# Kernel tuning notes

Hardware: AMD Instinct MI355X
Metric: run time of the kernel (lower is better)

The kernel has to match this reference:

```python
import jax, jax.numpy as jnp
import numpy as np

N_NODES = 50000
N_EDGES = 800000
F_IN = 128
HID = 128
HID4 = HID // 4  # 32
N_SEL = 8192


def gcn_conv(x, src, dst, norm, W, b, n_nodes):
    h = x @ W                              # [N, out]
    msg = h[src] * norm[:, None]           # gather + scale, [E+N, out]
    out = jax.ops.segment_sum(msg, dst, num_segments=n_nodes)  # scatter-add
    return out + b


def setup_inputs() -> dict:
    key = jax.random.key(0)
    ks = jax.random.split(key, 12)
    def glorot(k, shape):
        lim = np.sqrt(6.0 / (shape[0] + shape[1])).astype(np.float32)
        return jax.random.uniform(k, shape, jnp.float32, -lim, lim)
    return {
        "x": jax.random.normal(ks[0], (N_NODES, F_IN), jnp.float32),
        "edge_index": jax.random.randint(ks[1], (2, N_EDGES), 0, N_NODES, jnp.int64 if jax.config.jax_enable_x64 else jnp.int32),
        "relevant_batch_indices": jax.random.randint(ks[2], (N_SEL,), 0, N_NODES),
        "labels": jax.random.randint(ks[3], (N_SEL,), 0, 2),
        "W1": glorot(ks[4], (F_IN, HID)),   "b1": jnp.zeros((HID,), jnp.float32),
        "W2": glorot(ks[5], (HID, HID4)),   "b2": jnp.zeros((HID4,), jnp.float32),
        "W3": glorot(ks[6], (HID4, HID4)),  "b3": jnp.zeros((HID4,), jnp.float32),
        "Wl": glorot(ks[7], (HID4, 2)),     "bl": jnp.zeros((2,), jnp.float32),
    }


def reference(x, edge_index, relevant_batch_indices, labels, W1, b1, W2, b2, W3, b3, Wl, bl):
    n = x.shape[0]
    loops = jnp.arange(n, dtype=edge_index.dtype)
    src = jnp.concatenate([edge_index[0], loops])  # add self-loops
    dst = jnp.concatenate([edge_index[1], loops])
    deg = jax.ops.segment_sum(jnp.ones_like(dst, dtype=x.dtype), dst, num_segments=n)
    dis = jnp.where(deg > 0, jax.lax.rsqrt(jnp.maximum(deg, 1e-12)), 0.0)
    norm = dis[src] * dis[dst]             # [E+N]

    h = jax.nn.relu(gcn_conv(x, src, dst, norm, W1, b1, n))
    h = jax.nn.relu(gcn_conv(h, src, dst, norm, W2, b2, n))
    h = gcn_conv(h, src, dst, norm, W3, b3, n)

    logits = h[relevant_batch_indices] @ Wl + bl   # [N_SEL, 2]
    softmax_vals = jax.nn.softmax(logits, axis=1)
    lsm = jax.nn.log_softmax(logits, axis=1)
    # original slices lsm to labels length if longer; here shapes match
    lsm = lsm[: labels.shape[0]]
    return (lsm, softmax_vals)
```

## Files before the change

### kernel.cpp

```cpp
#include <hip/hip_runtime.h>
#include <hip/hip_fp16.h>

#define F_IN 128
#define HID 128
#define HID4 32
#define NPB 256
#define SRC_BITS 17
#define NBK 256
#define MAXBUCKET 256

static inline size_t alignup(size_t x) { return (x + 255) & ~(size_t)255; }

typedef _Float16 half8 __attribute__((ext_vector_type(8)));
typedef float f32x4 __attribute__((ext_vector_type(4)));

union F4H8 { float4 f; __half2 h[4]; };
union U2H4 { uint2 u; _Float16 h[4]; };


__global__ __launch_bounds__(1024) void hist_k(const int* __restrict__ dst,
                                               int* __restrict__ ghist, int ne, int n_buckets) {
    __shared__ int h[MAXBUCKET];
    const int t = threadIdx.x;
    for (int b = t; b < n_buckets; b += 1024) h[b] = 0;
    __syncthreads();
    const int chunk = (ne + NBK - 1) / NBK;
    const int beg = blockIdx.x * chunk;
    const int end = min(ne, beg + chunk);
    for (int e = beg + t; e < end; e += 1024)
        atomicAdd(&h[dst[e] / NPB], 1);
    __syncthreads();
    for (int b = t; b < n_buckets; b += 1024)
        ghist[(size_t)b * NBK + blockIdx.x] = h[b];
}


__global__ void scan_block_k(const int* __restrict__ in, int* __restrict__ out,
                             int* __restrict__ partials, int n) {
    __shared__ int tmp[256];
    int i = blockIdx.x * 256 + threadIdx.x;
    int v = (i < n) ? in[i] : 0;
    tmp[threadIdx.x] = v;
    __syncthreads();
    for (int off = 1; off < 256; off <<= 1) {
        int t = (threadIdx.x >= off) ? tmp[threadIdx.x - off] : 0;
        __syncthreads();
        tmp[threadIdx.x] += t;
        __syncthreads();
    }
    if (i < n) out[i] = tmp[threadIdx.x] - v;
    if (threadIdx.x == 255) partials[blockIdx.x] = tmp[255];
}

__global__ void scan_partials_k(int* __restrict__ partials, int nb) {
    __shared__ int tmp[256];
    int v = (threadIdx.x < nb) ? partials[threadIdx.x] : 0;
    tmp[threadIdx.x] = v;
    __syncthreads();
    for (int off = 1; off < 256; off <<= 1) {
        int t = (threadIdx.x >= off) ? tmp[threadIdx.x - off] : 0;
        __syncthreads();
        tmp[threadIdx.x] += t;
        __syncthreads();
    }
    if (threadIdx.x < nb) partials[threadIdx.x] = tmp[threadIdx.x] - v;
}

__global__ void add2_k(int* __restrict__ goff, const int* __restrict__ partials, int n) {
    int i = blockIdx.x * 256 + threadIdx.x;
    if (i < n) goff[i] += partials[i >> 8];
}


__global__ __launch_bounds__(1024) void scatter2_k(const int* __restrict__ src, const int* __restrict__ dst,
                                                   const int* __restrict__ goff,
                                                   unsigned* __restrict__ tmp, int ne, int n_buckets) {
    __shared__ int cur[MAXBUCKET];
    const int t = threadIdx.x;
    for (int b = t; b < n_buckets; b += 1024)
        cur[b] = goff[(size_t)b * NBK + blockIdx.x];
    __syncthreads();
    const int chunk = (ne + NBK - 1) / NBK;
    const int beg = blockIdx.x * chunk;
    const int end = min(ne, beg + chunk);
    for (int e = beg + t; e < end; e += 1024) {
        int d = dst[e];
        int s = src[e];
        int pos = atomicAdd(&cur[d / NPB], 1);
        tmp[pos] = ((unsigned)(d & (NPB - 1)) << SRC_BITS) | (unsigned)s;
    }
}


__global__ __launch_bounds__(NPB) void binC_k(const unsigned* __restrict__ tmp,
                                              const int* __restrict__ goff,
                                              int* __restrict__ deg, float* __restrict__ dis,
                                              int* __restrict__ rowoff, int* __restrict__ csr,
                                              int n_nodes, int ne, int n_buckets) {
    __shared__ int cnt[NPB];
    __shared__ int sc[NPB];
    const int t = threadIdx.x;
    const int bid = blockIdx.x;
    const int base = goff[(size_t)bid * NBK];
    const int end = (bid + 1 < n_buckets) ? goff[(size_t)(bid + 1) * NBK] : ne;

    cnt[t] = 0;
    __syncthreads();
    for (int j = base + t; j < end; j += NPB)
        atomicAdd(&cnt[tmp[j] >> SRC_BITS], 1);
    __syncthreads();

    int mydeg = cnt[t];
    sc[t] = mydeg;
    __syncthreads();
    for (int off = 1; off < NPB; off <<= 1) {
        int v = (t >= off) ? sc[t - off] : 0;
        __syncthreads();
        sc[t] += v;
        __syncthreads();
    }
    int excl = sc[t] - mydeg;
    int node = bid * NPB + t;
    if (node < n_nodes) {
        deg[node] = mydeg;
        dis[node] = rsqrtf((float)(mydeg + 1));
        rowoff[node] = base + excl;
    }
    cnt[t] = base + excl;
    __syncthreads();
    for (int j = base + t; j < end; j += NPB) {
        unsigned e = tmp[j];
        int ld = e >> SRC_BITS;
        int s  = e & ((1u << SRC_BITS) - 1);
        int pos = atomicAdd(&cnt[ld], 1);
        csr[pos] = s;
    }
}


__global__ void wprep_k(const float* __restrict__ W, _Float16* __restrict__ Wt) {
    int t = blockIdx.x * blockDim.x + threadIdx.x;
    if (t < 128 * 128) {
        int k = t >> 7, n = t & 127;
        Wt[n * 128 + k] = (_Float16)W[k * 128 + n];
    }
}


__global__ __launch_bounds__(256) void gemm1_mfma_k(const float* __restrict__ in,
                                                    const _Float16* __restrict__ Wt,
                                                    const float* __restrict__ dis,
                                                    __half* __restrict__ hout, int n_rows) {
    __shared__ _Float16 xs[64][136];
    __shared__ _Float16 wt[128][136];
    const int t = threadIdx.x;
    const int row0 = blockIdx.x * 64;

    #pragma unroll
    for (int i = 0; i < 8; ++i) {
        int q = t + i * 256;
        int row = q >> 5, c4 = (q & 31) * 4;
        float4 v = make_float4(0.f, 0.f, 0.f, 0.f);
        if (row0 + row < n_rows) v = *(const float4*)(in + (size_t)(row0 + row) * 128 + c4);
        U2H4 cv;
        cv.h[0] = (_Float16)v.x; cv.h[1] = (_Float16)v.y;
        cv.h[2] = (_Float16)v.z; cv.h[3] = (_Float16)v.w;
        *(uint2*)&xs[row][c4] = cv.u;
    }
    #pragma unroll
    for (int i = 0; i < 8; ++i) {
        int q = t + i * 256;
        int n = q >> 4, k0 = (q & 15) * 8;
        *(uint4*)&wt[n][k0] = *(const uint4*)(Wt + (size_t)n * 128 + k0);
    }
    __syncthreads();

    const int lane = t & 63;
    const int wave = t >> 6;
    const int r0 = wave * 16;
    const int lrow = lane & 15;
    const int kgrp = (lane >> 4) * 8;

    f32x4 acc[8];
    #pragma unroll
    for (int c = 0; c < 8; ++c) acc[c] = (f32x4){0.f, 0.f, 0.f, 0.f};

    #pragma unroll
    for (int kk = 0; kk < 4; ++kk) {
        const int k0 = kk * 32 + kgrp;
        half8 a = *(const half8*)&xs[r0 + lrow][k0];
        #pragma unroll
        for (int ct = 0; ct < 8; ++ct) {
            half8 b = *(const half8*)&wt[ct * 16 + lrow][k0];
            acc[ct] = __builtin_amdgcn_mfma_f32_16x16x32_f16(a, b, acc[ct], 0, 0, 0);
        }
    }

    const int rbase = row0 + r0 + (lane >> 4) * 4;
    #pragma unroll
    for (int i = 0; i < 4; ++i) {
        int row = rbase + i;
        if (row < n_rows) {
            float sc = dis[row];
            __half* p = hout + (size_t)row * 128 + lrow;
            #pragma unroll
            for (int ct = 0; ct < 8; ++ct)
                p[ct * 16] = __float2half(sc * acc[ct][i]);
        }
    }
}


__global__ __launch_bounds__(256) void gemm2_k(const float* __restrict__ in,
                                               const float* __restrict__ W,
                                               const float* __restrict__ dis,
                                               float* __restrict__ out, int n_rows) {
    __shared__ float xs[64][132];
    __shared__ float wt[128][32];
    const int t = threadIdx.x;
    const int row0 = blockIdx.x * 64;

    #pragma unroll
    for (int i = 0; i < 8; ++i) {
        int q = t + i * 256;
        int row = q >> 5, c4 = (q & 31) * 4;
        float4 v = make_float4(0.f, 0.f, 0.f, 0.f);
        if (row0 + row < n_rows) {
            v = *(const float4*)(in + (size_t)(row0 + row) * 128 + c4);
            v.x = fmaxf(v.x, 0.f); v.y = fmaxf(v.y, 0.f);
            v.z = fmaxf(v.z, 0.f); v.w = fmaxf(v.w, 0.f);
        }
        *(float4*)&xs[row][c4] = v;
    }
    #pragma unroll
    for (int i = 0; i < 4; ++i) {
        int q = t + i * 256;
        int kk = q >> 3, c4 = (q & 7) * 4;
        *(float4*)&wt[kk][c4] = *(const float4*)(W + (size_t)kk * 32 + c4);
    }
    __syncthreads();

    const int c4 = (t & 7) * 4;
    const int r2 = (t >> 3) * 2;

    float acc[2][4];
    #pragma unroll
    for (int i = 0; i < 2; ++i)
        #pragma unroll
        for (int j = 0; j < 4; ++j) acc[i][j] = 0.f;

    #pragma unroll 4
    for (int k = 0; k < 128; ++k) {
        float x0 = xs[r2][k], x1 = xs[r2 + 1][k];
        float4 w = *(float4*)&wt[k][c4];
        acc[0][0] += x0 * w.x; acc[0][1] += x0 * w.y; acc[0][2] += x0 * w.z; acc[0][3] += x0 * w.w;
        acc[1][0] += x1 * w.x; acc[1][1] += x1 * w.y; acc[1][2] += x1 * w.z; acc[1][3] += x1 * w.w;
    }

    #pragma unroll
    for (int i = 0; i < 2; ++i) {
        int row = row0 + r2 + i;
        if (row < n_rows) {
            float sc = dis[row];
            *(float4*)(out + (size_t)row * 32 + c4) =
                make_float4(sc * acc[i][0], sc * acc[i][1], sc * acc[i][2], sc * acc[i][3]);
        }
    }
}


__global__ __launch_bounds__(256) void gemm3_k(const float* __restrict__ in,
                                               const float* __restrict__ W,
                                               const float* __restrict__ dis,
                                               float* __restrict__ out, int n_rows) {
    __shared__ float xs[64][36];
    __shared__ float wt[32][32];
    const int t = threadIdx.x;
    const int row0 = blockIdx.x * 64;

    #pragma unroll
    for (int i = 0; i < 2; ++i) {
        int q = t + i * 256;
        int row = q >> 3, c4 = (q & 7) * 4;
        float4 v = make_float4(0.f, 0.f, 0.f, 0.f);
        if (row0 + row < n_rows) {
            v = *(const float4*)(in + (size_t)(row0 + row) * 32 + c4);
            v.x = fmaxf(v.x, 0.f); v.y = fmaxf(v.y, 0.f);
            v.z = fmaxf(v.z, 0.f); v.w = fmaxf(v.w, 0.f);
        }
        *(float4*)&xs[row][c4] = v;
    }
    {
        int kk = t >> 3, c4 = (t & 7) * 4;
        *(float4*)&wt[kk][c4] = *(const float4*)(W + (size_t)kk * 32 + c4);
    }
    __syncthreads();

    const int c4 = (t & 7) * 4;
    const int r2 = (t >> 3) * 2;

    float acc[2][4];
    #pragma unroll
    for (int i = 0; i < 2; ++i)
        #pragma unroll
        for (int j = 0; j < 4; ++j) acc[i][j] = 0.f;

    #pragma unroll
    for (int k = 0; k < 32; ++k) {
        float x0 = xs[r2][k], x1 = xs[r2 + 1][k];
        float4 w = *(float4*)&wt[k][c4];
        acc[0][0] += x0 * w.x; acc[0][1] += x0 * w.y; acc[0][2] += x0 * w.z; acc[0][3] += x0 * w.w;
        acc[1][0] += x1 * w.x; acc[1][1] += x1 * w.y; acc[1][2] += x1 * w.z; acc[1][3] += x1 * w.w;
    }

    #pragma unroll
    for (int i = 0; i < 2; ++i) {
        int row = row0 + r2 + i;
        if (row < n_rows) {
            float sc = dis[row];
            *(float4*)(out + (size_t)row * 32 + c4) =
                make_float4(sc * acc[i][0], sc * acc[i][1], sc * acc[i][2], sc * acc[i][3]);
        }
    }
}


__global__ void pull1_k(const __half* __restrict__ g, const int* __restrict__ rowoff,
                        const int* __restrict__ deg, const int* __restrict__ csr,
                        const float* __restrict__ dis, const float* __restrict__ b,
                        float* __restrict__ out, int n_nodes) {
    int gt = blockIdx.x * blockDim.x + threadIdx.x;
    int node = gt >> 4;
    int f0 = (gt & 15) * 8;
    if (node >= n_nodes) return;
    int beg = rowoff[node];
    int end = beg + deg[node];
    float dd = dis[node];

    float acc[8];
    {
        F4H8 v; v.f = *(const float4*)(g + (size_t)node * 128 + f0);
        #pragma unroll
        for (int k = 0; k < 4; ++k) {
            float2 p = __half22float2(v.h[k]);
            acc[2 * k] = p.x; acc[2 * k + 1] = p.y;
        }
    }

    int j = beg;
    for (; j + 2 <= end; j += 2) {
        int s0 = csr[j];
        int s1 = csr[j + 1];
        F4H8 v0; v0.f = *(const float4*)(g + (size_t)s0 * 128 + f0);
        F4H8 v1; v1.f = *(const float4*)(g + (size_t)s1 * 128 + f0);
        #pragma unroll
        for (int k = 0; k < 4; ++k) {
            float2 p0 = __half22float2(v0.h[k]);
            float2 p1 = __half22float2(v1.h[k]);
            acc[2 * k]     += p0.x + p1.x;
            acc[2 * k + 1] += p0.y + p1.y;
        }
    }
    if (j < end) {
        int s = csr[j];
        F4H8 v; v.f = *(const float4*)(g + (size_t)s * 128 + f0);
        #pragma unroll
        for (int k = 0; k < 4; ++k) {
            float2 p = __half22float2(v.h[k]);
            acc[2 * k] += p.x; acc[2 * k + 1] += p.y;
        }
    }

    float* o = out + (size_t)node * 128 + f0;
    float4 b0 = *(const float4*)(b + f0);
    float4 b1 = *(const float4*)(b + f0 + 4);
    *(float4*)o = make_float4(b0.x + dd * acc[0], b0.y + dd * acc[1],
                              b0.z + dd * acc[2], b0.w + dd * acc[3]);
    *(float4*)(o + 4) = make_float4(b1.x + dd * acc[4], b1.y + dd * acc[5],
                                    b1.z + dd * acc[6], b1.w + dd * acc[7]);
}


__global__ void pull2_k(const float* __restrict__ g, const int* __restrict__ rowoff,
                        const int* __restrict__ deg, const int* __restrict__ csr,
                        const float* __restrict__ dis, const float* __restrict__ b,
                        float* __restrict__ out, int n_nodes) {
    int gt = blockIdx.x * blockDim.x + threadIdx.x;
    int node = gt >> 3;
    int f0 = (gt & 7) * 4;
    if (node >= n_nodes) return;
    int beg = rowoff[node];
    int end = beg + deg[node];
    float dd = dis[node];

    float4 acc = *(const float4*)(g + (size_t)node * 32 + f0);

    int j = beg;
    for (; j + 2 <= end; j += 2) {
        int s0 = csr[j];
        int s1 = csr[j + 1];
        float4 h0 = *(const float4*)(g + (size_t)s0 * 32 + f0);
        float4 h1 = *(const float4*)(g + (size_t)s1 * 32 + f0);
        acc.x += h0.x + h1.x;
        acc.y += h0.y + h1.y;
        acc.z += h0.z + h1.z;
        acc.w += h0.w + h1.w;
    }
    if (j < end) {
        int s = csr[j];
        float4 hs = *(const float4*)(g + (size_t)s * 32 + f0);
        acc.x += hs.x; acc.y += hs.y; acc.z += hs.z; acc.w += hs.w;
    }

    float4 bb = *(const float4*)(b + f0);
    *(float4*)(out + (size_t)node * 32 + f0) =
        make_float4(bb.x + dd * acc.x, bb.y + dd * acc.y,
                    bb.z + dd * acc.z, bb.w + dd * acc.w);
}


__global__ void pull_head_k(const float* __restrict__ g, const int* __restrict__ rowoff,
                            const int* __restrict__ deg, const int* __restrict__ csr,
                            const float* __restrict__ dis, const float* __restrict__ b3,
                            const int* __restrict__ sel, const float* __restrict__ Wl,
                            const float* __restrict__ bl, float* __restrict__ out, int n_sel) {
    int gt = blockIdx.x * blockDim.x + threadIdx.x;
    int t = gt >> 3;
    int f0 = (gt & 7) * 4;
    if (t >= n_sel) return;
    int node = sel[t];
    int beg = rowoff[node];
    int end = beg + deg[node];
    float dd = dis[node];

    float4 acc = *(const float4*)(g + (size_t)node * 32 + f0);

    int j = beg;
    for (; j + 2 <= end; j += 2) {
        int s0 = csr[j];
        int s1 = csr[j + 1];
        float4 h0 = *(const float4*)(g + (size_t)s0 * 32 + f0);
        float4 h1 = *(const float4*)(g + (size_t)s1 * 32 + f0);
        acc.x += h0.x + h1.x;
        acc.y += h0.y + h1.y;
        acc.z += h0.z + h1.z;
        acc.w += h0.w + h1.w;
    }
    if (j < end) {
        int s = csr[j];
        float4 hs = *(const float4*)(g + (size_t)s * 32 + f0);
        acc.x += hs.x; acc.y += hs.y; acc.z += hs.z; acc.w += hs.w;
    }

    float4 bb = *(const float4*)(b3 + f0);
    float a0 = bb.x + dd * acc.x;
    float a1 = bb.y + dd * acc.y;
    float a2 = bb.z + dd * acc.z;
    float a3 = bb.w + dd * acc.w;

    float l0 = a0 * Wl[(f0 + 0) * 2] + a1 * Wl[(f0 + 1) * 2]
             + a2 * Wl[(f0 + 2) * 2] + a3 * Wl[(f0 + 3) * 2];
    float l1 = a0 * Wl[(f0 + 0) * 2 + 1] + a1 * Wl[(f0 + 1) * 2 + 1]
             + a2 * Wl[(f0 + 2) * 2 + 1] + a3 * Wl[(f0 + 3) * 2 + 1];
    #pragma unroll
    for (int m = 1; m < 8; m <<= 1) {
        l0 += __shfl_xor(l0, m);
        l1 += __shfl_xor(l1, m);
    }
    if ((gt & 7) == 0) {
        l0 += bl[0]; l1 += bl[1];
        float mx = fmaxf(l0, l1);
        float e0 = expf(l0 - mx), e1 = expf(l1 - mx);
        float s = e0 + e1;
        float ls = logf(s);
        *(float2*)(out + (size_t)t * 2) = make_float2((l0 - mx) - ls, (l1 - mx) - ls);
        *(float2*)(out + 2 * (size_t)n_sel + (size_t)t * 2) = make_float2(e0 / s, e1 / s);
    }
}


extern "C" void kernel_launch(void* const* d_in, const int* in_sizes, int n_in,
                              void* d_out, int out_size, void* d_ws, size_t ws_size,
                              hipStream_t stream) {
    const float* x  = (const float*)d_in[0];
    const int* edge = (const int*)d_in[1];
    const int* sel  = (const int*)d_in[2];
    const float* W1 = (const float*)d_in[4];
    const float* b1 = (const float*)d_in[5];
    const float* W2 = (const float*)d_in[6];
    const float* b2 = (const float*)d_in[7];
    const float* W3 = (const float*)d_in[8];
    const float* b3 = (const float*)d_in[9];
    const float* Wl = (const float*)d_in[10];
    const float* bl = (const float*)d_in[11];
    float* out = (float*)d_out;

    const int n_nodes = in_sizes[0] / F_IN;
    const int n_edges = in_sizes[1] / 2;
    const int n_sel   = in_sizes[2];
    const int* srcv = edge;
    const int* dstv = edge + n_edges;
    const int n_buckets = (n_nodes + NPB - 1) / NPB;
    const int n_gh = n_buckets * NBK;

    char* ws = (char*)d_ws;
    int*       deg      = (int*)ws;       ws += alignup((size_t)n_nodes * 4);
    float*     dis      = (float*)ws;     ws += alignup((size_t)n_nodes * 4);
    int*       rowoff   = (int*)ws;       ws += alignup((size_t)n_nodes * 4);
    int*       ghist    = (int*)ws;       ws += alignup((size_t)n_gh * 4);
    int*       goff     = (int*)ws;       ws += alignup((size_t)n_gh * 4);
    int*       partial2 = (int*)ws;       ws += alignup(1024);
    _Float16*  Wt       = (_Float16*)ws;  ws += alignup(128 * 128 * 2);
    unsigned*  tmp      = (unsigned*)ws;  ws += alignup((size_t)n_edges * 4);
    int*       csr      = (int*)ws;       ws += alignup((size_t)n_edges * 4);
    char*      bufA     = ws;             ws += alignup((size_t)n_nodes * HID * 4);
    float*     bufB     = (float*)ws;

    const int B = 256;
    #define GRD(n) (((n) + B - 1) / B)
    const int nblk2 = GRD(n_gh);

    hist_k<<<NBK, 1024, 0, stream>>>(dstv, ghist, n_edges, n_buckets);
    scan_block_k<<<nblk2, B, 0, stream>>>(ghist, goff, partial2, n_gh);
    scan_partials_k<<<1, B, 0, stream>>>(partial2, nblk2);
    add2_k<<<nblk2, B, 0, stream>>>(goff, partial2, n_gh);
    scatter2_k<<<NBK, 1024, 0, stream>>>(srcv, dstv, goff, tmp, n_edges, n_buckets);
    binC_k<<<n_buckets, NPB, 0, stream>>>(tmp, goff, deg, dis, rowoff, csr, n_nodes, n_edges, n_buckets);

    const int gemm_blocks = (n_nodes + 63) / 64;

    wprep_k<<<GRD(128 * 128), B, 0, stream>>>(W1, Wt);
    gemm1_mfma_k<<<gemm_blocks, B, 0, stream>>>(x, Wt, dis, (__half*)bufA, n_nodes);
    pull1_k<<<GRD(n_nodes * 16), B, 0, stream>>>((const __half*)bufA, rowoff, deg, csr, dis, b1, bufB, n_nodes);

    gemm2_k<<<gemm_blocks, B, 0, stream>>>(bufB, W2, dis, (float*)bufA, n_nodes);
    pull2_k<<<GRD(n_nodes * 8), B, 0, stream>>>((const float*)bufA, rowoff, deg, csr, dis, b2, bufB, n_nodes);

    gemm3_k<<<gemm_blocks, B, 0, stream>>>(bufB, W3, dis, (float*)bufA, n_nodes);
    pull_head_k<<<GRD(n_sel * 8), B, 0, stream>>>((const float*)bufA, rowoff, deg, csr, dis, b3,
                                                  sel, Wl, bl, out, n_sel);

    #undef GRD
}
```

Baseline: 139.3 us.

## Fold small prep kernels into neighbors, store layer-2 features as fp16, read W1 directly

The W1 transpose and fp16 conversion moves into the histogram kernel, and the add2 scan-fixup kernel is dropped. Scatter and bin kernels now add the partial sums themselves, which removes two launches. gemm1 reads weight fragments straight from global memory instead of staging them in LDS. gemm2 writes fp16 output and pull2 gathers it as fp16, halving the bytes of the layer-2 gather at some cost in precision. Relying on hist_k finishing before gemm1 is fine on one stream, but the uncached global weight reads inside the MFMA loop could add latency.

```diff
diff --git a/kernel.cpp b/kernel.cpp
--- a/kernel.cpp
+++ b/kernel.cpp
@@ -16,12 +16,21 @@
 
 union F4H8 { float4 f; __half2 h[4]; };
 union U2H4 { uint2 u; _Float16 h[4]; };
+union UH2  { unsigned u; __half2 h; };
 
 
 __global__ __launch_bounds__(1024) void hist_k(const int* __restrict__ dst,
-                                               int* __restrict__ ghist, int ne, int n_buckets) {
+                                               int* __restrict__ ghist,
+                                               const float* __restrict__ W1,
+                                               _Float16* __restrict__ Wt,
+                                               int ne, int n_buckets) {
     __shared__ int h[MAXBUCKET];
     const int t = threadIdx.x;
+    if (blockIdx.x < 16) {
+        int q = blockIdx.x * 1024 + t;
+        int k = q >> 7, n = q & 127;
+        Wt[n * 128 + k] = (_Float16)W1[q];
+    }
     for (int b = t; b < n_buckets; b += 1024) h[b] = 0;
     __syncthreads();
     const int chunk = (ne + NBK - 1) / NBK;
@@ -66,19 +75,15 @@
     if (threadIdx.x < nb) partials[threadIdx.x] = tmp[threadIdx.x] - v;
 }
 
-__global__ void add2_k(int* __restrict__ goff, const int* __restrict__ partials, int n) {
-    int i = blockIdx.x * 256 + threadIdx.x;
-    if (i < n) goff[i] += partials[i >> 8];
-}
-
 
 __global__ __launch_bounds__(1024) void scatter2_k(const int* __restrict__ src, const int* __restrict__ dst,
                                                    const int* __restrict__ goff,
+                                                   const int* __restrict__ partial2,
                                                    unsigned* __restrict__ tmp, int ne, int n_buckets) {
     __shared__ int cur[MAXBUCKET];
     const int t = threadIdx.x;
     for (int b = t; b < n_buckets; b += 1024)
-        cur[b] = goff[(size_t)b * NBK + blockIdx.x];
+        cur[b] = goff[(size_t)b * NBK + blockIdx.x] + partial2[b];
     __syncthreads();
     const int chunk = (ne + NBK - 1) / NBK;
     const int beg = blockIdx.x * chunk;
@@ -94,6 +99,7 @@
 
 __global__ __launch_bounds__(NPB) void binC_k(const unsigned* __restrict__ tmp,
                                               const int* __restrict__ goff,
+                                              const int* __restrict__ partial2,
                                               int* __restrict__ deg, float* __restrict__ dis,
                                               int* __restrict__ rowoff, int* __restrict__ csr,
                                               int n_nodes, int ne, int n_buckets) {
@@ -101,8 +107,8 @@
     __shared__ int sc[NPB];
     const int t = threadIdx.x;
     const int bid = blockIdx.x;
-    const int base = goff[(size_t)bid * NBK];
-    const int end = (bid + 1 < n_buckets) ? goff[(size_t)(bid + 1) * NBK] : ne;
+    const int base = goff[(size_t)bid * NBK] + partial2[bid];
+    const int end = (bid + 1 < n_buckets) ? goff[(size_t)(bid + 1) * NBK] + partial2[bid + 1] : ne;
 
     cnt[t] = 0;
     __syncthreads();
@@ -138,21 +144,11 @@
 }
 
 
-__global__ void wprep_k(const float* __restrict__ W, _Float16* __restrict__ Wt) {
-    int t = blockIdx.x * blockDim.x + threadIdx.x;
-    if (t < 128 * 128) {
-        int k = t >> 7, n = t & 127;
-        Wt[n * 128 + k] = (_Float16)W[k * 128 + n];
-    }
-}
-
-
 __global__ __launch_bounds__(256) void gemm1_mfma_k(const float* __restrict__ in,
                                                     const _Float16* __restrict__ Wt,
                                                     const float* __restrict__ dis,
                                                     __half* __restrict__ hout, int n_rows) {
     __shared__ _Float16 xs[64][136];
-    __shared__ _Float16 wt[128][136];
     const int t = threadIdx.x;
     const int row0 = blockIdx.x * 64;
 
@@ -167,12 +163,6 @@
         cv.h[2] = (_Float16)v.z; cv.h[3] = (_Float16)v.w;
         *(uint2*)&xs[row][c4] = cv.u;
     }
-    #pragma unroll
-    for (int i = 0; i < 8; ++i) {
-        int q = t + i * 256;
-        int n = q >> 4, k0 = (q & 15) * 8;
-        *(uint4*)&wt[n][k0] = *(const uint4*)(Wt + (size_t)n * 128 + k0);
-    }
     __syncthreads();
 
     const int lane = t & 63;
@@ -191,7 +181,7 @@
         half8 a = *(const half8*)&xs[r0 + lrow][k0];
         #pragma unroll
         for (int ct = 0; ct < 8; ++ct) {
-            half8 b = *(const half8*)&wt[ct * 16 + lrow][k0];
+            half8 b = *(const half8*)(Wt + (size_t)(ct * 16 + lrow) * 128 + k0);
             acc[ct] = __builtin_amdgcn_mfma_f32_16x16x32_f16(a, b, acc[ct], 0, 0, 0);
         }
     }
@@ -206,120 +196,6 @@
             #pragma unroll
             for (int ct = 0; ct < 8; ++ct)
                 p[ct * 16] = __float2half(sc * acc[ct][i]);
-        }
-    }
-}
-
-
-__global__ __launch_bounds__(256) void gemm2_k(const float* __restrict__ in,
-                                               const float* __restrict__ W,
-                                               const float* __restrict__ dis,
-                                               float* __restrict__ out, int n_rows) {
-    __shared__ float xs[64][132];
-    __shared__ float wt[128][32];
-    const int t = threadIdx.x;
-    const int row0 = blockIdx.x * 64;
-
-    #pragma unroll
-    for (int i = 0; i < 8; ++i) {
-        int q = t + i * 256;
-        int row = q >> 5, c4 = (q & 31) * 4;
-        float4 v = make_float4(0.f, 0.f, 0.f, 0.f);
-        if (row0 + row < n_rows) {
-            v = *(const float4*)(in + (size_t)(row0 + row) * 128 + c4);
-            v.x = fmaxf(v.x, 0.f); v.y = fmaxf(v.y, 0.f);
-            v.z = fmaxf(v.z, 0.f); v.w = fmaxf(v.w, 0.f);
-        }
-        *(float4*)&xs[row][c4] = v;
-    }
-    #pragma unroll
-    for (int i = 0; i < 4; ++i) {
-        int q = t + i * 256;
-        int kk = q >> 3, c4 = (q & 7) * 4;
-        *(float4*)&wt[kk][c4] = *(const float4*)(W + (size_t)kk * 32 + c4);
-    }
-    __syncthreads();
-
-    const int c4 = (t & 7) * 4;
-    const int r2 = (t >> 3) * 2;
-
-    float acc[2][4];
-    #pragma unroll
-    for (int i = 0; i < 2; ++i)
-        #pragma unroll
-        for (int j = 0; j < 4; ++j) acc[i][j] = 0.f;
-
-    #pragma unroll 4
-    for (int k = 0; k < 128; ++k) {
-        float x0 = xs[r2][k], x1 = xs[r2 + 1][k];
-        float4 w = *(float4*)&wt[k][c4];
-        acc[0][0] += x0 * w.x; acc[0][1] += x0 * w.y; acc[0][2] += x0 * w.z; acc[0][3] += x0 * w.w;
-        acc[1][0] += x1 * w.x; acc[1][1] += x1 * w.y; acc[1][2] += x1 * w.z; acc[1][3] += x1 * w.w;
-    }
-
-    #pragma unroll
-    for (int i = 0; i < 2; ++i) {
-        int row = row0 + r2 + i;
-        if (row < n_rows) {
-            float sc = dis[row];
-            *(float4*)(out + (size_t)row * 32 + c4) =
-                make_float4(sc * acc[i][0], sc * acc[i][1], sc * acc[i][2], sc * acc[i][3]);
-        }
-    }
-}
-
-
-__global__ __launch_bounds__(256) void gemm3_k(const float* __restrict__ in,
-                                               const float* __restrict__ W,
-                                               const float* __restrict__ dis,
-                                               float* __restrict__ out, int n_rows) {
-    __shared__ float xs[64][36];
-    __shared__ float wt[32][32];
-    const int t = threadIdx.x;
-    const int row0 = blockIdx.x * 64;
-
-    #pragma unroll
-    for (int i = 0; i < 2; ++i) {
-        int q = t + i * 256;
-        int row = q >> 3, c4 = (q & 7) * 4;
-        float4 v = make_float4(0.f, 0.f, 0.f, 0.f);
-        if (row0 + row < n_rows) {
-            v = *(const float4*)(in + (size_t)(row0 + row) * 32 + c4);
-            v.x = fmaxf(v.x, 0.f); v.y = fmaxf(v.y, 0.f);
-            v.z = fmaxf(v.z, 0.f); v.w = fmaxf(v.w, 0.f);
-        }
-        *(float4*)&xs[row][c4] = v;
-    }
-    {
-        int kk = t >> 3, c4 = (t & 7) * 4;
-        *(float4*)&wt[kk][c4] = *(const float4*)(W + (size_t)kk * 32 + c4);
-    }
-    __syncthreads();
-
-    const int c4 = (t & 7) * 4;
-    const int r2 = (t >> 3) * 2;
-
-    float acc[2][4];
-    #pragma unroll
-    for (int i = 0; i < 2; ++i)
-        #pragma unroll
-        for (int j = 0; j < 4; ++j) acc[i][j] = 0.f;
-
-    #pragma unroll
-    for (int k = 0; k < 32; ++k) {
-        float x0 = xs[r2][k], x1 = xs[r2 + 1][k];
-        float4 w = *(float4*)&wt[k][c4];
-        acc[0][0] += x0 * w.x; acc[0][1] += x0 * w.y; acc[0][2] += x0 * w.z; acc[0][3] += x0 * w.w;
-        acc[1][0] += x1 * w.x; acc[1][1] += x1 * w.y; acc[1][2] += x1 * w.z; acc[1][3] += x1 * w.w;
-    }
-
-    #pragma unroll
-    for (int i = 0; i < 2; ++i) {
-        int row = row0 + r2 + i;
-        if (row < n_rows) {
-            float sc = dis[row];
-            *(float4*)(out + (size_t)row * 32 + c4) =
-                make_float4(sc * acc[i][0], sc * acc[i][1], sc * acc[i][2], sc * acc[i][3]);
         }
     }
 }
@@ -381,7 +257,69 @@
 }
 
 
-__global__ void pull2_k(const float* __restrict__ g, const int* __restrict__ rowoff,
+__global__ __launch_bounds__(256) void gemm2_k(const float* __restrict__ in,
+                                               const float* __restrict__ W,
+                                               const float* __restrict__ dis,
+                                               __half* __restrict__ out, int n_rows) {
+    __shared__ float xs[64][132];
+    __shared__ float wt[128][32];
+    const int t = threadIdx.x;
+    const int row0 = blockIdx.x * 64;
+
+    #pragma unroll
+    for (int i = 0; i < 8; ++i) {
+        int q = t + i * 256;
+        int row = q >> 5, c4 = (q & 31) * 4;
+        float4 v = make_float4(0.f, 0.f, 0.f, 0.f);
+        if (row0 + row < n_rows) {
+            v = *(const float4*)(in + (size_t)(row0 + row) * 128 + c4);
+            v.x = fmaxf(v.x, 0.f); v.y = fmaxf(v.y, 0.f);
+            v.z = fmaxf(v.z, 0.f); v.w = fmaxf(v.w, 0.f);
+        }
+        *(float4*)&xs[row][c4] = v;
+    }
+    #pragma unroll
+    for (int i = 0; i < 4; ++i) {
+        int q = t + i * 256;
+        int kk = q >> 3, c4 = (q & 7) * 4;
+        *(float4*)&wt[kk][c4] = *(const float4*)(W + (size_t)kk * 32 + c4);
+    }
+    __syncthreads();
+
+    const int c4 = (t & 7) * 4;
+    const int r2 = (t >> 3) * 2;
+
+    float acc[2][4];
+    #pragma unroll
+    for (int i = 0; i < 2; ++i)
+        #pragma unroll
+        for (int j = 0; j < 4; ++j) acc[i][j] = 0.f;
+
+    #pragma unroll 4
+    for (int k = 0; k < 128; ++k) {
+        float x0 = xs[r2][k], x1 = xs[r2 + 1][k];
+        float4 w = *(float4*)&wt[k][c4];
+        acc[0][0] += x0 * w.x; acc[0][1] += x0 * w.y; acc[0][2] += x0 * w.z; acc[0][3] += x0 * w.w;
+        acc[1][0] += x1 * w.x; acc[1][1] += x1 * w.y; acc[1][2] += x1 * w.z; acc[1][3] += x1 * w.w;
+    }
+
+    #pragma unroll
+    for (int i = 0; i < 2; ++i) {
+        int row = row0 + r2 + i;
+        if (row < n_rows) {
+            float sc = dis[row];
+            U2H4 cv;
+            cv.h[0] = (_Float16)(sc * acc[i][0]);
+            cv.h[1] = (_Float16)(sc * acc[i][1]);
+            cv.h[2] = (_Float16)(sc * acc[i][2]);
+            cv.h[3] = (_Float16)(sc * acc[i][3]);
+            *(uint2*)(out + (size_t)row * 32 + c4) = cv.u;
+        }
+    }
+}
+
+
+__global__ void pull2_k(const __half* __restrict__ g, const int* __restrict__ rowoff,
                         const int* __restrict__ deg, const int* __restrict__ csr,
                         const float* __restrict__ dis, const float* __restrict__ b,
                         float* __restrict__ out, int n_nodes) {
@@ -393,29 +331,89 @@
     int end = beg + deg[node];
     float dd = dis[node];
 
-    float4 acc = *(const float4*)(g + (size_t)node * 32 + f0);
+    float acc[4];
+    {
+        U2H4 v; v.u = *(const uint2*)(g + (size_t)node * 32 + f0);
+        #pragma unroll
+        for (int k = 0; k < 4; ++k) acc[k] = (float)v.h[k];
+    }
 
     int j = beg;
     for (; j + 2 <= end; j += 2) {
         int s0 = csr[j];
         int s1 = csr[j + 1];
-        float4 h0 = *(const float4*)(g + (size_t)s0 * 32 + f0);
-        float4 h1 = *(const float4*)(g + (size_t)s1 * 32 + f0);
-        acc.x += h0.x + h1.x;
-        acc.y += h0.y + h1.y;
-        acc.z += h0.z + h1.z;
-        acc.w += h0.w + h1.w;
+        U2H4 v0; v0.u = *(const uint2*)(g + (size_t)s0 * 32 + f0);
+        U2H4 v1; v1.u = *(const uint2*)(g + (size_t)s1 * 32 + f0);
+        #pragma unroll
+        for (int k = 0; k < 4; ++k) acc[k] += (float)v0.h[k] + (float)v1.h[k];
     }
     if (j < end) {
         int s = csr[j];
-        float4 hs = *(const float4*)(g + (size_t)s * 32 + f0);
-        acc.x += hs.x; acc.y += hs.y; acc.z += hs.z; acc.w += hs.w;
+        U2H4 v; v.u = *(const uint2*)(g + (size_t)s * 32 + f0);
+        #pragma unroll
+        for (int k = 0; k < 4; ++k) acc[k] += (float)v.h[k];
     }
 
     float4 bb = *(const float4*)(b + f0);
     *(float4*)(out + (size_t)node * 32 + f0) =
-        make_float4(bb.x + dd * acc.x, bb.y + dd * acc.y,
-                    bb.z + dd * acc.z, bb.w + dd * acc.w);
+        make_float4(bb.x + dd * acc[0], bb.y + dd * acc[1],
+                    bb.z + dd * acc[2], bb.w + dd * acc[3]);
+}
+
+
+__global__ __launch_bounds__(256) void gemm3_k(const float* __restrict__ in,
+                                               const float* __restrict__ W,
+                                               const float* __restrict__ dis,
+                                               float* __restrict__ out, int n_rows) {
+    __shared__ float xs[64][36];
+    __shared__ float wt[32][32];
+    const int t = threadIdx.x;
+    const int row0 = blockIdx.x * 64;
+
+    #pragma unroll
+    for (int i = 0; i < 2; ++i) {
+        int q = t + i * 256;
+        int row = q >> 3, c4 = (q & 7) * 4;
+        float4 v = make_float4(0.f, 0.f, 0.f, 0.f);
+        if (row0 + row < n_rows) {
+            v = *(const float4*)(in + (size_t)(row0 + row) * 32 + c4);
+            v.x = fmaxf(v.x, 0.f); v.y = fmaxf(v.y, 0.f);
+            v.z = fmaxf(v.z, 0.f); v.w = fmaxf(v.w, 0.f);
+        }
+        *(float4*)&xs[row][c4] = v;
+    }
+    {
+        int kk = t >> 3, c4 = (t & 7) * 4;
+        *(float4*)&wt[kk][c4] = *(const float4*)(W + (size_t)kk * 32 + c4);
+    }
+    __syncthreads();
+
+    const int c4 = (t & 7) * 4;
+    const int r2 = (t >> 3) * 2;
+
+    float acc[2][4];
+    #pragma unroll
+    for (int i = 0; i < 2; ++i)
+        #pragma unroll
+        for (int j = 0; j < 4; ++j) acc[i][j] = 0.f;
+
+    #pragma unroll
+    for (int k = 0; k < 32; ++k) {
+        float x0 = xs[r2][k], x1 = xs[r2 + 1][k];
+        float4 w = *(float4*)&wt[k][c4];
+        acc[0][0] += x0 * w.x; acc[0][1] += x0 * w.y; acc[0][2] += x0 * w.z; acc[0][3] += x0 * w.w;
+        acc[1][0] += x1 * w.x; acc[1][1] += x1 * w.y; acc[1][2] += x1 * w.z; acc[1][3] += x1 * w.w;
+    }
+
+    #pragma unroll
+    for (int i = 0; i < 2; ++i) {
+        int row = row0 + r2 + i;
+        if (row < n_rows) {
+            float sc = dis[row];
+            *(float4*)(out + (size_t)row * 32 + c4) =
+                make_float4(sc * acc[i][0], sc * acc[i][1], sc * acc[i][2], sc * acc[i][3]);
+        }
+    }
 }
 
 
@@ -520,21 +518,20 @@
     #define GRD(n) (((n) + B - 1) / B)
     const int nblk2 = GRD(n_gh);
 
-    hist_k<<<NBK, 1024, 0, stream>>>(dstv, ghist, n_edges, n_buckets);
+    hist_k<<<NBK, 1024, 0, stream>>>(dstv, ghist, W1, Wt, n_edges, n_buckets);
     scan_block_k<<<nblk2, B, 0, stream>>>(ghist, goff, partial2, n_gh);
     scan_partials_k<<<1, B, 0, stream>>>(partial2, nblk2);
-    add2_k<<<nblk2, B, 0, stream>>>(goff, partial2, n_gh);
-    scatter2_k<<<NBK, 1024, 0, stream>>>(srcv, dstv, goff, tmp, n_edges, n_buckets);
-    binC_k<<<n_buckets, NPB, 0, stream>>>(tmp, goff, deg, dis, rowoff, csr, n_nodes, n_edges, n_buckets);
+    scatter2_k<<<NBK, 1024, 0, stream>>>(srcv, dstv, goff, partial2, tmp, n_edges, n_buckets);
+    binC_k<<<n_buckets, NPB, 0, stream>>>(tmp, goff, partial2, deg, dis, rowoff, csr,
+                                          n_nodes, n_edges, n_buckets);
 
     const int gemm_blocks = (n_nodes + 63) / 64;
 
-    wprep_k<<<GRD(128 * 128), B, 0, stream>>>(W1, Wt);
     gemm1_mfma_k<<<gemm_blocks, B, 0, stream>>>(x, Wt, dis, (__half*)bufA, n_nodes);
     pull1_k<<<GRD(n_nodes * 16), B, 0, stream>>>((const __half*)bufA, rowoff, deg, csr, dis, b1, bufB, n_nodes);
 
-    gemm2_k<<<gemm_blocks, B, 0, stream>>>(bufB, W2, dis, (float*)bufA, n_nodes);
-    pull2_k<<<GRD(n_nodes * 8), B, 0, stream>>>((const float*)bufA, rowoff, deg, csr, dis, b2, bufB, n_nodes);
+    gemm2_k<<<gemm_blocks, B, 0, stream>>>(bufB, W2, dis, (__half*)bufA, n_nodes);
+    pull2_k<<<GRD(n_nodes * 8), B, 0, stream>>>((const __half*)bufA, rowoff, deg, csr, dis, b2, bufB, n_nodes);
 
     gemm3_k<<<gemm_blocks, B, 0, stream>>>(bufB, W3, dis, (float*)bufA, n_nodes);
     pull_head_k<<<GRD(n_sel * 8), B, 0, stream>>>((const float*)bufA, rowoff, deg, csr, dis, b3,
```

After: 139.1 us. No clear change (-0.1%).
